# Performance work log

Measured on AMD Instinct MI355X. Metric: run time of the kernel, lower is better.

The kernel has to match this reference:

```python
import jax, jax.numpy as jnp
import numpy as np

N_NODES = 50000


def _cluster_gcn_conv(x, row, col, W_out, b_out, W_root, num_nodes):
    # PyG ClusterGCNConv with diag_lambda=0.0 and self-loops already added.
    deg = jax.ops.segment_sum(jnp.ones_like(col, dtype=x.dtype), col,
                              num_segments=num_nodes)
    deg_inv = 1.0 / jnp.clip(deg, 1.0)
    w = deg_inv[col]                       # [E_total]
    msg = x[row] * w[:, None]              # [E_total, d] gather + scale
    agg = jax.ops.segment_sum(msg, col, num_segments=num_nodes)  # scatter-add
    return agg @ W_out + b_out + x @ W_root


def setup_inputs() -> dict:
    key = jax.random.key(0)
    ks = jax.random.split(key, 12)
    N, E, d_in, d_h, d_out = N_NODES, 800000, 128, 128, 64
    x = jax.random.normal(ks[0], (N, d_in), dtype=jnp.float32)
    edge_index = jax.random.randint(ks[1], (2, E), 0, N, dtype=jnp.int64)
    s = lambda fan_in: 1.0 / np.sqrt(fan_in)
    return {
        "x": x,
        "edge_index": edge_index,
        "W1_out": jax.random.normal(ks[2], (d_in, d_h), jnp.float32) * s(d_in),
        "b1": jnp.zeros((d_h,), jnp.float32),
        "W1_root": jax.random.normal(ks[3], (d_in, d_h), jnp.float32) * s(d_in),
        "W2_out": jax.random.normal(ks[4], (d_h, d_h), jnp.float32) * s(d_h),
        "b2": jnp.zeros((d_h,), jnp.float32),
        "W2_root": jax.random.normal(ks[5], (d_h, d_h), jnp.float32) * s(d_h),
        "W3_out": jax.random.normal(ks[6], (d_h, d_out), jnp.float32) * s(d_h),
        "b3": jnp.zeros((d_out,), jnp.float32),
        "W3_root": jax.random.normal(ks[7], (d_h, d_out), jnp.float32) * s(d_h),
    }


def reference(x, edge_index, W1_out, b1, W1_root, W2_out, b2, W2_root,
              W3_out, b3, W3_root):
    N = x.shape[0]
    loops = jnp.arange(N, dtype=edge_index.dtype)
    row = jnp.concatenate([edge_index[0], loops])  # add self loops
    col = jnp.concatenate([edge_index[1], loops])
    # layer 1 + relu (dropout is identity at inference)
    x = jax.nn.relu(_cluster_gcn_conv(x, row, col, W1_out, b1, W1_root, N))
    # layer 2 + relu
    x = jax.nn.relu(_cluster_gcn_conv(x, row, col, W2_out, b2, W2_root, N))
    # layer 3 + relu, then log_softmax (no pooling: node classification)
    x = jax.nn.relu(_cluster_gcn_conv(x, row, col, W3_out, b3, W3_root, N))
    return jax.nn.log_softmax(x, axis=-1)
```

## Files before the change

kernel.cpp:

```cpp
#include <hip/hip_runtime.h>
#include <math.h>


constexpr int DK = 128;
constexpr int NBUCK = 256;
constexpr int ESTRIDE = 3584;
constexpr int EPB = 2048;

typedef __attribute__((ext_vector_type(8))) short bf16x8;
typedef __attribute__((ext_vector_type(4))) float f32x4;

__device__ inline unsigned short f2bf(float f) {
    unsigned int u; __builtin_memcpy(&u, &f, 4);
    unsigned int r = (u + 0x7FFFu + ((u >> 16) & 1u)) >> 16;
    return (unsigned short)r;
}
__device__ inline float blo(unsigned int u) {
    unsigned int t = u << 16; float f; __builtin_memcpy(&f, &t, 4); return f;
}
__device__ inline float bhi(unsigned int u) {
    unsigned int t = u & 0xffff0000u; float f; __builtin_memcpy(&f, &t, 4); return f;
}

__device__ void wprep_body(const float* __restrict__ Wout, const float* __restrict__ Wroot,
                           uint4* __restrict__ frag, int dout, int tid) {
    int total = 8 * (dout >> 4) * 64;
    if (tid >= total) return;
    int L = tid & 63;
    int fu = (tid >> 6) % (dout >> 4);
    int t = (tid >> 6) / (dout >> 4);
    int quad = L >> 4, l15 = L & 15;
    int n = fu * 16 + l15;
    unsigned int p[4];
#pragma unroll
    for (int jj = 0; jj < 4; ++jj) {
        int k0 = t * 32 + quad * 8 + jj * 2;
        float v0 = (k0 < 128) ? Wout[k0 * dout + n] : Wroot[(k0 - 128) * dout + n];
        int k1 = k0 + 1;
        float v1 = (k1 < 128) ? Wout[k1 * dout + n] : Wroot[(k1 - 128) * dout + n];
        p[jj] = (unsigned)f2bf(v0) | ((unsigned)f2bf(v1) << 16);
    }
    frag[tid] = make_uint4(p[0], p[1], p[2], p[3]);
}

__global__ void k_prep(const float4* __restrict__ x, uint2* __restrict__ xb,
                       const int* __restrict__ row, const int* __restrict__ col,
                       int* __restrict__ bcnt, unsigned int* __restrict__ ebuf,
                       int n4, int E, int bspan, int npart,
                       const float* __restrict__ W1o, const float* __restrict__ W1r, uint4* wf1,
                       const float* __restrict__ W2o, const float* __restrict__ W2r, uint4* wf2,
                       const float* __restrict__ W3o, const float* __restrict__ W3r, uint4* wf3) {
    const int b = blockIdx.x;
    const int tid = threadIdx.x;
    if (b < npart) {
        __shared__ int cnt[NBUCK];
        __shared__ int base[NBUCK];
        const int t0 = b * EPB;
        cnt[tid] = 0;
        __syncthreads();
        int bk[EPB / 256];
#pragma unroll
        for (int k = 0; k < EPB / 256; ++k) {
            int i = t0 + k * 256 + tid;
            int bb = -1;
            if (i < E) { bb = col[i] / bspan; atomicAdd(&cnt[bb], 1); }
            bk[k] = bb;
        }
        __syncthreads();
        base[tid] = cnt[tid] ? atomicAdd(&bcnt[tid], cnt[tid]) : 0;
        cnt[tid] = 0;
        __syncthreads();
#pragma unroll
        for (int k = 0; k < EPB / 256; ++k) {
            int i = t0 + k * 256 + tid;
            if (i < E) {
                int bb = bk[k];
                int gpos = base[bb] + atomicAdd(&cnt[bb], 1);
                if (gpos < ESTRIDE) {
                    unsigned int colofs = (unsigned)(col[i] - bb * bspan);
                    ebuf[(size_t)bb * ESTRIDE + gpos] =
                        ((unsigned)row[i] & 0xFFFFu) | (colofs << 16);
                }
            }
        }
    } else if (b < npart + 16) {
        wprep_body(W1o, W1r, wf1, 128, (b - npart) * 256 + tid);
    } else if (b < npart + 32) {
        wprep_body(W2o, W2r, wf2, 128, (b - npart - 16) * 256 + tid);
    } else if (b < npart + 40) {
        wprep_body(W3o, W3r, wf3, 64, (b - npart - 32) * 256 + tid);
    } else {
        int i = (b - npart - 40) * 256 + tid;
        if (i >= n4) return;
        float4 v = x[i];
        uint2 o;
        o.x = (unsigned)f2bf(v.x) | ((unsigned)f2bf(v.y) << 16);
        o.y = (unsigned)f2bf(v.z) | ((unsigned)f2bf(v.w) << 16);
        xb[i] = o;
    }
}

__global__ __launch_bounds__(512)
void k_fillb(const unsigned int* __restrict__ ebuf,
             const int* __restrict__ bcnt, int* __restrict__ offs,
             float* __restrict__ deginv, unsigned short* __restrict__ srow,
             int n, int bspan) {
    __shared__ int cnt[4096];
    __shared__ int scan_s[NBUCK + 1];
    __shared__ int wsum[4];
    const int b = blockIdx.x, tid = threadIdx.x;
    const int lane = tid & 63, wid = tid >> 6;

    int v = 0, ps = 0;
    if (tid < 256) {
        v = min(bcnt[tid], ESTRIDE);
        ps = v;
#pragma unroll
        for (int off = 1; off < 64; off <<= 1) {
            int t = __shfl_up(ps, off);
            if (lane >= off) ps += t;
        }
        if (lane == 63) wsum[wid] = ps;
    }
    __syncthreads();
    if (tid < 256) {
        int wb = 0;
        for (int w = 0; w < wid; ++w) wb += wsum[w];
        int excl = wb + ps - v;
        scan_s[tid] = excl;
        if (tid == 255) scan_s[256] = excl + v;
    }
    for (int i = tid; i < 4096; i += 512) cnt[i] = 0;
    __syncthreads();

    const int cntb = min(bcnt[b], ESTRIDE);
    const int csr0 = scan_s[b];
    if (b == NBUCK - 1 && tid == 0) offs[n] = scan_s[256];
    const size_t eb0 = (size_t)b * ESTRIDE;
    for (int i = tid; i < cntb; i += 512) {
        const unsigned u = ebuf[eb0 + i];
        atomicAdd(&cnt[(int)(u >> 16) * 16 + (int)((u & 0xFFFFu) >> 12)], 1);
    }
    __syncthreads();

    int vv[16], s = 0, ps2 = 0;
    if (tid < 256) {
#pragma unroll
        for (int r = 0; r < 16; ++r) { vv[r] = cnt[tid * 16 + r]; s += vv[r]; }
        ps2 = s;
#pragma unroll
        for (int off = 1; off < 64; off <<= 1) {
            int t = __shfl_up(ps2, off);
            if (lane >= off) ps2 += t;
        }
        if (lane == 63) wsum[wid] = ps2;
    }
    __syncthreads();
    if (tid < 256) {
        int wb = 0;
        for (int w = 0; w < wid; ++w) wb += wsum[w];
        int excl = csr0 + wb + ps2 - s;
        const int node = b * bspan + tid;
        if (tid < bspan && node < n) {
            offs[node] = excl;
            deginv[node] = 1.0f / (float)(s + 1);
        }
#pragma unroll
        for (int r = 0; r < 16; ++r) { int t = vv[r]; cnt[tid * 16 + r] = excl; excl += t; }
    }
    __syncthreads();
    for (int i = tid; i < cntb; i += 512) {
        const unsigned u = ebuf[eb0 + i];
        const int pos = atomicAdd(&cnt[(int)(u >> 16) * 16 + (int)((u & 0xFFFFu) >> 12)], 1);
        srow[pos] = (unsigned short)(u & 0xFFFFu);
    }
}

template <bool HR>
__global__ __launch_bounds__(256, 5)
void k_fused(const unsigned short* __restrict__ xb,
             const int* __restrict__ offs, const unsigned short* __restrict__ srow,
             const float* __restrict__ deginv,
             const uint4* __restrict__ wfrag, const float* __restrict__ bvec,
             unsigned short* __restrict__ y,
             const uint4* __restrict__ wfrag3, const float* __restrict__ b3,
             unsigned short* __restrict__ H, float* __restrict__ R, int n) {
    __shared__ unsigned short At[32][136];
    __shared__ unsigned short sIdx[768];
    const int tid = threadIdx.x;
    const int m0 = blockIdx.x * 32;
    const uint4* __restrict__ xb4 = (const uint4*)xb;

    const int s0 = offs[m0];
    const int eAll = offs[min(m0 + 32, n)];
    const int cntE = eAll - s0;
    const bool staged = (cntE <= 768);
    for (int i = tid; i < cntE && i < 768; i += 256) sIdx[i] = srow[s0 + i];
    __syncthreads();
    const unsigned short* __restrict__ idxp = staged ? sIdx : srow;
    const int bias = staged ? s0 : 0;

#pragma unroll
    for (int rnd = 0; rnd < 2; ++rnd) {
        const int nl = rnd * 16 + (tid >> 4);
        const int lane = tid & 15;
        const int node = m0 + nl;
        if (node < n) {
            const size_t rb = (size_t)node * 16 + lane;
            uint4 sv = xb4[rb];
            float a0 = blo(sv.x), a1 = bhi(sv.x), a2 = blo(sv.y), a3 = bhi(sv.y);
            float a4 = blo(sv.z), a5 = bhi(sv.z), a6 = blo(sv.w), a7 = bhi(sv.w);
            const int s = offs[node] - bias, e = offs[node + 1] - bias;
            int p = s;
            for (; p + 4 <= e; p += 4) {
                const int r0 = idxp[p], r1 = idxp[p + 1];
                const int r2 = idxp[p + 2], r3 = idxp[p + 3];
                const uint4 v0 = xb4[(size_t)r0 * 16 + lane];
                const uint4 v1 = xb4[(size_t)r1 * 16 + lane];
                const uint4 v2 = xb4[(size_t)r2 * 16 + lane];
                const uint4 v3 = xb4[(size_t)r3 * 16 + lane];
                a0 += (blo(v0.x) + blo(v1.x)) + (blo(v2.x) + blo(v3.x));
                a1 += (bhi(v0.x) + bhi(v1.x)) + (bhi(v2.x) + bhi(v3.x));
                a2 += (blo(v0.y) + blo(v1.y)) + (blo(v2.y) + blo(v3.y));
                a3 += (bhi(v0.y) + bhi(v1.y)) + (bhi(v2.y) + bhi(v3.y));
                a4 += (blo(v0.z) + blo(v1.z)) + (blo(v2.z) + blo(v3.z));
                a5 += (bhi(v0.z) + bhi(v1.z)) + (bhi(v2.z) + bhi(v3.z));
                a6 += (blo(v0.w) + blo(v1.w)) + (blo(v2.w) + blo(v3.w));
                a7 += (bhi(v0.w) + bhi(v1.w)) + (bhi(v2.w) + bhi(v3.w));
            }
            for (; p < e; ++p) {
                const uint4 v = xb4[(size_t)idxp[p] * 16 + lane];
                a0 += blo(v.x); a1 += bhi(v.x); a2 += blo(v.y); a3 += bhi(v.y);
                a4 += blo(v.z); a5 += bhi(v.z); a6 += blo(v.w); a7 += bhi(v.w);
            }
            const float w = deginv[node];
            uint4 o;
            o.x = (unsigned)f2bf(a0 * w) | ((unsigned)f2bf(a1 * w) << 16);
            o.y = (unsigned)f2bf(a2 * w) | ((unsigned)f2bf(a3 * w) << 16);
            o.z = (unsigned)f2bf(a4 * w) | ((unsigned)f2bf(a5 * w) << 16);
            o.w = (unsigned)f2bf(a6 * w) | ((unsigned)f2bf(a7 * w) << 16);
            *(uint4*)&At[nl][lane * 8] = o;
        }
    }
    __syncthreads();

    const int w = tid >> 6, L = tid & 63;
    const int quad = L >> 4, l15 = L & 15;

    f32x4 acc[2][2];
#pragma unroll
    for (int mt = 0; mt < 2; ++mt)
#pragma unroll
        for (int u = 0; u < 2; ++u)
            acc[mt][u] = (f32x4){0.f, 0.f, 0.f, 0.f};

    const bf16x8 zf = {0, 0, 0, 0, 0, 0, 0, 0};
#pragma unroll
    for (int t = 0; t < 8; ++t) {
        bf16x8 bfr[2];
#pragma unroll
        for (int u = 0; u < 2; ++u)
            bfr[u] = *(const bf16x8*)&wfrag[(size_t)((t * 8 + (w * 2 + u)) * 64 + L)];
        const int koff = (t & 3) * 32 + quad * 8;
        bf16x8 af[2];
#pragma unroll
        for (int mt = 0; mt < 2; ++mt) {
            const int rl = mt * 16 + l15;
            if (t < 4) {
                af[mt] = *(const bf16x8*)&At[rl][koff];
            } else {
                const int r = m0 + rl;
                af[mt] = (r < n) ? *(const bf16x8*)(xb + (size_t)r * 128 + koff) : zf;
            }
        }
#pragma unroll
        for (int mt = 0; mt < 2; ++mt)
#pragma unroll
            for (int u = 0; u < 2; ++u)
                acc[mt][u] = __builtin_amdgcn_mfma_f32_16x16x32_bf16(
                    af[mt], bfr[u], acc[mt][u], 0, 0, 0);
    }

    float bb[2];
    bb[0] = bvec[w * 32 + l15];
    bb[1] = bvec[w * 32 + 16 + l15];

    if (!HR) {
#pragma unroll
        for (int mt = 0; mt < 2; ++mt)
#pragma unroll
            for (int u = 0; u < 2; ++u)
#pragma unroll
                for (int r4 = 0; r4 < 4; ++r4) {
                    const int r = m0 + mt * 16 + quad * 4 + r4;
                    if (r < n) {
                        float v = fmaxf(acc[mt][u][r4] + bb[u], 0.f);
                        y[(size_t)r * 128 + w * 32 + u * 16 + l15] = f2bf(v);
                    }
                }
        return;
    }

    __syncthreads();
#pragma unroll
    for (int mt = 0; mt < 2; ++mt)
#pragma unroll
        for (int u = 0; u < 2; ++u)
#pragma unroll
            for (int r4 = 0; r4 < 4; ++r4) {
                const int rl = mt * 16 + quad * 4 + r4;
                float v = fmaxf(acc[mt][u][r4] + bb[u], 0.f);
                At[rl][w * 32 + u * 16 + l15] = f2bf(v);
            }
    __syncthreads();

    f32x4 accH[2], accR[2];
#pragma unroll
    for (int mt = 0; mt < 2; ++mt) {
        accH[mt] = (f32x4){0.f, 0.f, 0.f, 0.f};
        accR[mt] = (f32x4){0.f, 0.f, 0.f, 0.f};
    }
#pragma unroll
    for (int t = 0; t < 4; ++t) {
        const bf16x8 bo = *(const bf16x8*)&wfrag3[(size_t)((t * 4 + w) * 64 + L)];
        const bf16x8 br = *(const bf16x8*)&wfrag3[(size_t)(((t + 4) * 4 + w) * 64 + L)];
        const int koff = t * 32 + quad * 8;
        bf16x8 af[2];
#pragma unroll
        for (int mt = 0; mt < 2; ++mt)
            af[mt] = *(const bf16x8*)&At[mt * 16 + l15][koff];
#pragma unroll
        for (int mt = 0; mt < 2; ++mt) {
            accH[mt] = __builtin_amdgcn_mfma_f32_16x16x32_bf16(af[mt], bo, accH[mt], 0, 0, 0);
            accR[mt] = __builtin_amdgcn_mfma_f32_16x16x32_bf16(af[mt], br, accR[mt], 0, 0, 0);
        }
    }
    const float bb3 = b3[w * 16 + l15];
#pragma unroll
    for (int mt = 0; mt < 2; ++mt)
#pragma unroll
        for (int r4 = 0; r4 < 4; ++r4) {
            const int r = m0 + mt * 16 + quad * 4 + r4;
            if (r < n) {
                H[(size_t)r * 64 + w * 16 + l15] = f2bf(accH[mt][r4]);
                R[(size_t)r * 64 + w * 16 + l15] = accR[mt][r4] + bb3;
            }
        }
}

__global__ __launch_bounds__(256, 8)
void k_gather3(const uint2* __restrict__ Hb, const float4* __restrict__ R4,
               const int* __restrict__ offs, const unsigned short* __restrict__ srow,
               const float* __restrict__ deginv, float4* __restrict__ out, int n) {
    __shared__ unsigned short sIdx[512];
    const int tid = threadIdx.x;
    const int m0 = blockIdx.x * 16;
    const int s0 = offs[m0];
    const int eAll = offs[min(m0 + 16, n)];
    const int cntE = eAll - s0;
    const bool staged = (cntE <= 512);
    for (int i = tid; i < cntE && i < 512; i += 256) sIdx[i] = srow[s0 + i];
    __syncthreads();
    const unsigned short* __restrict__ idxp = staged ? sIdx : srow;
    const int bias = staged ? s0 : 0;

    const int node = m0 + (tid >> 4);
    const int lane = tid & 15;
    if (node >= n) return;
    const size_t rb = (size_t)node * 16 + lane;
    uint2 sv = Hb[rb];
    float a0 = blo(sv.x), a1 = bhi(sv.x), a2 = blo(sv.y), a3 = bhi(sv.y);
    const int s = offs[node] - bias, e = offs[node + 1] - bias;
    int p = s;
    for (; p + 4 <= e; p += 4) {
        const int r0 = idxp[p], r1 = idxp[p + 1], r2 = idxp[p + 2], r3 = idxp[p + 3];
        const uint2 v0 = Hb[(size_t)r0 * 16 + lane];
        const uint2 v1 = Hb[(size_t)r1 * 16 + lane];
        const uint2 v2 = Hb[(size_t)r2 * 16 + lane];
        const uint2 v3 = Hb[(size_t)r3 * 16 + lane];
        a0 += (blo(v0.x) + blo(v1.x)) + (blo(v2.x) + blo(v3.x));
        a1 += (bhi(v0.x) + bhi(v1.x)) + (bhi(v2.x) + bhi(v3.x));
        a2 += (blo(v0.y) + blo(v1.y)) + (blo(v2.y) + blo(v3.y));
        a3 += (bhi(v0.y) + bhi(v1.y)) + (bhi(v2.y) + bhi(v3.y));
    }
    for (; p < e; ++p) {
        const uint2 v = Hb[(size_t)idxp[p] * 16 + lane];
        a0 += blo(v.x); a1 += bhi(v.x); a2 += blo(v.y); a3 += bhi(v.y);
    }
    const float w = deginv[node];
    const float4 r = R4[rb];
    float v0 = fmaxf(a0 * w + r.x, 0.f);
    float v1 = fmaxf(a1 * w + r.y, 0.f);
    float v2 = fmaxf(a2 * w + r.z, 0.f);
    float v3 = fmaxf(a3 * w + r.w, 0.f);
    float m = fmaxf(fmaxf(v0, v1), fmaxf(v2, v3));
    m = fmaxf(m, __shfl_xor(m, 1));
    m = fmaxf(m, __shfl_xor(m, 2));
    m = fmaxf(m, __shfl_xor(m, 4));
    m = fmaxf(m, __shfl_xor(m, 8));
    float s2 = __expf(v0 - m) + __expf(v1 - m) + __expf(v2 - m) + __expf(v3 - m);
    s2 += __shfl_xor(s2, 1);
    s2 += __shfl_xor(s2, 2);
    s2 += __shfl_xor(s2, 4);
    s2 += __shfl_xor(s2, 8);
    const float lse = m + __logf(s2);
    out[rb] = make_float4(v0 - lse, v1 - lse, v2 - lse, v3 - lse);
}

extern "C" void kernel_launch(void* const* d_in, const int* in_sizes, int n_in,
                              void* d_out, int out_size, void* d_ws, size_t ws_size,
                              hipStream_t stream) {
    const float* x   = (const float*)d_in[0];
    const int*   ei  = (const int*)d_in[1];
    const float* W1o = (const float*)d_in[2];
    const float* b1  = (const float*)d_in[3];
    const float* W1r = (const float*)d_in[4];
    const float* W2o = (const float*)d_in[5];
    const float* b2  = (const float*)d_in[6];
    const float* W2r = (const float*)d_in[7];
    const float* W3o = (const float*)d_in[8];
    const float* b3  = (const float*)d_in[9];
    const float* W3r = (const float*)d_in[10];

    const int N = in_sizes[0] / DK;
    const int E = in_sizes[1] / 2;
    const int* row = ei;
    const int* col = ei + E;
    const int bspan = (N + NBUCK - 1) / NBUCK;

    int*   bcnt   = (int*)d_ws;
    int*   offs   = bcnt + 256;
    float* deginv = (float*)(offs + ((N + 64) & ~63));
    unsigned short* srow = (unsigned short*)(deginv + ((N + 63) & ~63));
    unsigned int* ebuf = (unsigned int*)(srow + ((E + 63) & ~63));
    uint4* wf1    = (uint4*)(ebuf + (size_t)NBUCK * ESTRIDE);
    uint4* wf2    = wf1 + 4096;
    uint4* wf3    = wf2 + 4096;
    unsigned short* xbuf = (unsigned short*)(wf3 + 2048);
    unsigned short* Ya   = xbuf + (size_t)N * 128;
    unsigned short* Hb   = Ya + (size_t)N * 128;
    float* Rb = (float*)(Hb + (size_t)N * 64);
    float* out = (float*)d_out;

    const int n4 = N * 32;
    const int nxblk = (n4 + 255) / 256;
    const int npart = (E + EPB - 1) / EPB;

    hipMemsetAsync(bcnt, 0, NBUCK * sizeof(int), stream);
    k_prep<<<npart + 40 + nxblk, 256, 0, stream>>>((const float4*)x, (uint2*)xbuf,
                                                   row, col, bcnt, ebuf,
                                                   n4, E, bspan, npart,
                                                   W1o, W1r, wf1, W2o, W2r, wf2,
                                                   W3o, W3r, wf3);
    k_fillb<<<NBUCK, 512, 0, stream>>>(ebuf, bcnt, offs, deginv, srow, N, bspan);

    const int Gf = (N + 31) / 32;
    const int Gg3 = (N + 15) / 16;

    k_fused<false><<<Gf, 256, 0, stream>>>(xbuf, offs, srow, deginv, wf1, b1, Ya,
                                           nullptr, nullptr, nullptr, nullptr, N);
    k_fused<true><<<Gf, 256, 0, stream>>>(Ya, offs, srow, deginv, wf2, b2, nullptr,
                                          wf3, b3, Hb, Rb, N);
    k_gather3<<<Gg3, 256, 0, stream>>>((const uint2*)Hb, (const float4*)Rb,
                                       offs, srow, deginv, (float4*)out, N);
}
```

Before: 208.1 us.

## Halve node tile per block and stage self features in shared memory

Fused GEMM kernels now process 16 nodes per block instead of 32. Each node's own feature row, already loaded for the self-loop term, is kept in a shared-memory tile, so the root GEMM operand no longer needs a second global read. The final gather kernel uses 128-thread blocks covering 8 nodes, and launch bounds are raised to allow more resident blocks. The aim is more parallelism and occupancy for the latency-bound gathers, at the cost of fewer MFMA per weight-fragment load and twice as many blocks.

```diff
diff --git a/kernel.cpp b/kernel.cpp
--- a/kernel.cpp
+++ b/kernel.cpp
@@ -177,7 +177,7 @@
 }
 
 template <bool HR>
-__global__ __launch_bounds__(256, 5)
+__global__ __launch_bounds__(256, 8)
 void k_fused(const unsigned short* __restrict__ xb,
              const int* __restrict__ offs, const unsigned short* __restrict__ srow,
              const float* __restrict__ deginv,
@@ -185,29 +185,30 @@
              unsigned short* __restrict__ y,
              const uint4* __restrict__ wfrag3, const float* __restrict__ b3,
              unsigned short* __restrict__ H, float* __restrict__ R, int n) {
-    __shared__ unsigned short At[32][136];
-    __shared__ unsigned short sIdx[768];
+    __shared__ unsigned short At[16][136];
+    __shared__ unsigned short Xt[16][136];
+    __shared__ unsigned short sIdx[512];
     const int tid = threadIdx.x;
-    const int m0 = blockIdx.x * 32;
+    const int m0 = blockIdx.x * 16;
     const uint4* __restrict__ xb4 = (const uint4*)xb;
 
     const int s0 = offs[m0];
-    const int eAll = offs[min(m0 + 32, n)];
+    const int eAll = offs[min(m0 + 16, n)];
     const int cntE = eAll - s0;
-    const bool staged = (cntE <= 768);
-    for (int i = tid; i < cntE && i < 768; i += 256) sIdx[i] = srow[s0 + i];
+    const bool staged = (cntE <= 512);
+    for (int i = tid; i < cntE && i < 512; i += 256) sIdx[i] = srow[s0 + i];
     __syncthreads();
     const unsigned short* __restrict__ idxp = staged ? sIdx : srow;
     const int bias = staged ? s0 : 0;
 
-#pragma unroll
-    for (int rnd = 0; rnd < 2; ++rnd) {
-        const int nl = rnd * 16 + (tid >> 4);
+    {
+        const int nl = tid >> 4;
         const int lane = tid & 15;
         const int node = m0 + nl;
         if (node < n) {
             const size_t rb = (size_t)node * 16 + lane;
             uint4 sv = xb4[rb];
+            *(uint4*)&Xt[nl][lane * 8] = sv;
             float a0 = blo(sv.x), a1 = bhi(sv.x), a2 = blo(sv.y), a3 = bhi(sv.y);
             float a4 = blo(sv.z), a5 = bhi(sv.z), a6 = blo(sv.w), a7 = bhi(sv.w);
             const int s = offs[node] - bias, e = offs[node + 1] - bias;
@@ -247,14 +248,10 @@
     const int w = tid >> 6, L = tid & 63;
     const int quad = L >> 4, l15 = L & 15;
 
-    f32x4 acc[2][2];
-#pragma unroll
-    for (int mt = 0; mt < 2; ++mt)
-#pragma unroll
-        for (int u = 0; u < 2; ++u)
-            acc[mt][u] = (f32x4){0.f, 0.f, 0.f, 0.f};
-
-    const bf16x8 zf = {0, 0, 0, 0, 0, 0, 0, 0};
+    f32x4 acc[2];
+    acc[0] = (f32x4){0.f, 0.f, 0.f, 0.f};
+    acc[1] = (f32x4){0.f, 0.f, 0.f, 0.f};
+
 #pragma unroll
     for (int t = 0; t < 8; ++t) {
         bf16x8 bfr[2];
@@ -262,23 +259,11 @@
         for (int u = 0; u < 2; ++u)
             bfr[u] = *(const bf16x8*)&wfrag[(size_t)((t * 8 + (w * 2 + u)) * 64 + L)];
         const int koff = (t & 3) * 32 + quad * 8;
-        bf16x8 af[2];
-#pragma unroll
-        for (int mt = 0; mt < 2; ++mt) {
-            const int rl = mt * 16 + l15;
-            if (t < 4) {
-                af[mt] = *(const bf16x8*)&At[rl][koff];
-            } else {
-                const int r = m0 + rl;
-                af[mt] = (r < n) ? *(const bf16x8*)(xb + (size_t)r * 128 + koff) : zf;
-            }
-        }
-#pragma unroll
-        for (int mt = 0; mt < 2; ++mt)
-#pragma unroll
-            for (int u = 0; u < 2; ++u)
-                acc[mt][u] = __builtin_amdgcn_mfma_f32_16x16x32_bf16(
-                    af[mt], bfr[u], acc[mt][u], 0, 0, 0);
+        const bf16x8 af = (t < 4) ? *(const bf16x8*)&At[l15][koff]
+                                  : *(const bf16x8*)&Xt[l15][koff];
+#pragma unroll
+        for (int u = 0; u < 2; ++u)
+            acc[u] = __builtin_amdgcn_mfma_f32_16x16x32_bf16(af, bfr[u], acc[u], 0, 0, 0);
     }
 
     float bb[2];
@@ -287,79 +272,63 @@
 
     if (!HR) {
 #pragma unroll
-        for (int mt = 0; mt < 2; ++mt)
-#pragma unroll
-            for (int u = 0; u < 2; ++u)
-#pragma unroll
-                for (int r4 = 0; r4 < 4; ++r4) {
-                    const int r = m0 + mt * 16 + quad * 4 + r4;
-                    if (r < n) {
-                        float v = fmaxf(acc[mt][u][r4] + bb[u], 0.f);
-                        y[(size_t)r * 128 + w * 32 + u * 16 + l15] = f2bf(v);
-                    }
+        for (int u = 0; u < 2; ++u)
+#pragma unroll
+            for (int r4 = 0; r4 < 4; ++r4) {
+                const int r = m0 + quad * 4 + r4;
+                if (r < n) {
+                    float v = fmaxf(acc[u][r4] + bb[u], 0.f);
+                    y[(size_t)r * 128 + w * 32 + u * 16 + l15] = f2bf(v);
                 }
+            }
         return;
     }
 
     __syncthreads();
 #pragma unroll
-    for (int mt = 0; mt < 2; ++mt)
-#pragma unroll
-        for (int u = 0; u < 2; ++u)
-#pragma unroll
-            for (int r4 = 0; r4 < 4; ++r4) {
-                const int rl = mt * 16 + quad * 4 + r4;
-                float v = fmaxf(acc[mt][u][r4] + bb[u], 0.f);
-                At[rl][w * 32 + u * 16 + l15] = f2bf(v);
-            }
-    __syncthreads();
-
-    f32x4 accH[2], accR[2];
-#pragma unroll
-    for (int mt = 0; mt < 2; ++mt) {
-        accH[mt] = (f32x4){0.f, 0.f, 0.f, 0.f};
-        accR[mt] = (f32x4){0.f, 0.f, 0.f, 0.f};
-    }
+    for (int u = 0; u < 2; ++u)
+#pragma unroll
+        for (int r4 = 0; r4 < 4; ++r4) {
+            const int rl = quad * 4 + r4;
+            float v = fmaxf(acc[u][r4] + bb[u], 0.f);
+            At[rl][w * 32 + u * 16 + l15] = f2bf(v);
+        }
+    __syncthreads();
+
+    f32x4 accH = (f32x4){0.f, 0.f, 0.f, 0.f};
+    f32x4 accR = (f32x4){0.f, 0.f, 0.f, 0.f};
 #pragma unroll
     for (int t = 0; t < 4; ++t) {
         const bf16x8 bo = *(const bf16x8*)&wfrag3[(size_t)((t * 4 + w) * 64 + L)];
         const bf16x8 br = *(const bf16x8*)&wfrag3[(size_t)(((t + 4) * 4 + w) * 64 + L)];
         const int koff = t * 32 + quad * 8;
-        bf16x8 af[2];
-#pragma unroll
-        for (int mt = 0; mt < 2; ++mt)
-            af[mt] = *(const bf16x8*)&At[mt * 16 + l15][koff];
-#pragma unroll
-        for (int mt = 0; mt < 2; ++mt) {
-            accH[mt] = __builtin_amdgcn_mfma_f32_16x16x32_bf16(af[mt], bo, accH[mt], 0, 0, 0);
-            accR[mt] = __builtin_amdgcn_mfma_f32_16x16x32_bf16(af[mt], br, accR[mt], 0, 0, 0);
-        }
+        const bf16x8 af = *(const bf16x8*)&At[l15][koff];
+        accH = __builtin_amdgcn_mfma_f32_16x16x32_bf16(af, bo, accH, 0, 0, 0);
+        accR = __builtin_amdgcn_mfma_f32_16x16x32_bf16(af, br, accR, 0, 0, 0);
     }
     const float bb3 = b3[w * 16 + l15];
 #pragma unroll
-    for (int mt = 0; mt < 2; ++mt)
-#pragma unroll
-        for (int r4 = 0; r4 < 4; ++r4) {
-            const int r = m0 + mt * 16 + quad * 4 + r4;
-            if (r < n) {
-                H[(size_t)r * 64 + w * 16 + l15] = f2bf(accH[mt][r4]);
-                R[(size_t)r * 64 + w * 16 + l15] = accR[mt][r4] + bb3;
-            }
-        }
-}
-
-__global__ __launch_bounds__(256, 8)
+    for (int r4 = 0; r4 < 4; ++r4) {
+        const int r = m0 + quad * 4 + r4;
+        if (r < n) {
+            H[(size_t)r * 64 + w * 16 + l15] = f2bf(accH[r4]);
+            R[(size_t)r * 64 + w * 16 + l15] = accR[r4] + bb3;
+        }
+    }
+}
+
+__global__ __launch_bounds__(128, 16)
 void k_gather3(const uint2* __restrict__ Hb, const float4* __restrict__ R4,
                const int* __restrict__ offs, const unsigned short* __restrict__ srow,
                const float* __restrict__ deginv, float4* __restrict__ out, int n) {
-    __shared__ unsigned short sIdx[512];
+    __shared__ unsigned short sIdx[256];
     const int tid = threadIdx.x;
-    const int m0 = blockIdx.x * 16;
+    const int m0 = blockIdx.x * 8;
     const int s0 = offs[m0];
-    const int eAll = offs[min(m0 + 16, n)];
+    const int eAll = offs[min(m0 + 8, n)];
     const int cntE = eAll - s0;
-    const bool staged = (cntE <= 512);
-    for (int i = tid; i < cntE && i < 512; i += 256) sIdx[i] = srow[s0 + i];
+    const bool staged = (cntE <= 256);
+    for (int i = tid; i < cntE && i < 256; i += 128) sIdx[i] = srow[s0 + i];
     __syncthreads();
     const unsigned short* __restrict__ idxp = staged ? sIdx : srow;
     const int bias = staged ? s0 : 0;
@@ -454,13 +423,13 @@
                                                    W3o, W3r, wf3);
     k_fillb<<<NBUCK, 512, 0, stream>>>(ebuf, bcnt, offs, deginv, srow, N, bspan);
 
-    const int Gf = (N + 31) / 32;
-    const int Gg3 = (N + 15) / 16;
+    const int Gf = (N + 15) / 16;
+    const int Gg3 = (N + 7) / 8;
 
     k_fused<false><<<Gf, 256, 0, stream>>>(xbuf, offs, srow, deginv, wf1, b1, Ya,
                                            nullptr, nullptr, nullptr, nullptr, N);
     k_fused<true><<<Gf, 256, 0, stream>>>(Ya, offs, srow, deginv, wf2, b2, nullptr,
                                           wf3, b3, Hb, Rb, N);
-    k_gather3<<<Gg3, 256, 0, stream>>>((const uint2*)Hb, (const float4*)Rb,
+    k_gather3<<<Gg3, 128, 0, stream>>>((const uint2*)Hb, (const float4*)Rb,
                                        offs, srow, deginv, (float4*)out, N);
 }
```

After: 201.0 us. 3.4% less time.
